# Kernel optimization log

Measured on AMD Instinct MI355X. Metric: run time of the kernel, lower is better.

Reference implementation:

```python
import jax, jax.numpy as jnp
import numpy as np
import math

B, A, I, O = 4096, 32, 256, 256


def setup_inputs() -> dict:
    key = jax.random.key(0)
    kx, kw, kb = jax.random.split(key, 3)
    x = jax.random.normal(kx, (B, A, I), dtype=jnp.float32)
    # kaiming_uniform_(a=sqrt(5)) on [A, O, I]: fan_in = I, bound = sqrt(6/((1+5)*I)) = 1/sqrt(I)
    wb = 1.0 / math.sqrt(I)
    weight = jax.random.uniform(kw, (A, O, I), minval=-wb, maxval=wb, dtype=jnp.float32)
    bb = 1.0 / math.sqrt(I)
    bias = jax.random.uniform(kb, (A, O), minval=-bb, maxval=bb, dtype=jnp.float32)
    return {"x": x, "weight": weight, "bias": bias}


def reference(x, weight, bias):
    # per-assignment batched GEMM: weight [A,O,I], x [B,A,I] -> [B,A,O]
    return jnp.einsum('aoi,bai->bao', weight, x) + bias
```

## Files before the change

### kernel.cpp

```cpp
#include <hip/hip_runtime.h>

typedef __attribute__((ext_vector_type(4))) float f32x4;
typedef __attribute__((ext_vector_type(2))) unsigned u32x2;
typedef __attribute__((ext_vector_type(8))) short bf16x8;

constexpr int Bsz = 4096, Asz = 32, Isz = 256, Osz = 256;
constexpr int NI = 16;

__device__ inline unsigned cvtpk(float lo, float hi) {
    unsigned r;
    asm("v_cvt_pk_bf16_f32 %0, %1, %2" : "=v"(r) : "v"(lo), "v"(hi));
    return r;
}

__global__ __launch_bounds__(512, 2) void al_gemm(const float* __restrict__ x,
                                                  const float* __restrict__ wsrc,
                                                  const float* __restrict__ bias,
                                                  float* __restrict__ out)
{
    __shared__ char sA[2][16384];
    __shared__ char sB[131072];

    const int p  = blockIdx.x;
    const int a  = (p & 7) * 4 + ((p >> 3) & 3);
    const int b0 = (p >> 5) * 512;

    const int t    = threadIdx.x;
    const int w    = t >> 6;
    const int lane = t & 63;
    const int llo  = lane & 15, lhi = lane >> 4;

    const float* fs[4];
    int wadr[4];
#pragma unroll
    for (int j = 0; j < 4; ++j) {
        const int lr = 4 * w + j;
        fs[j]   = x + ((size_t)(b0 + lr) * Asz + a) * Isz + lane * 4;
        wadr[j] = lr * 512 + (((lane >> 1) ^ lr) << 4) + (lane & 1) * 8;
    }
    const size_t STEP = (size_t)32 * Asz * Isz;

    f32x4 LA[4], LB[4];

#define FISSUE(Lset, tn) {                                                     \
    const size_t o_ = (size_t)(tn) * STEP;                                     \
    _Pragma("unroll")                                                          \
    for (int j = 0; j < 4; ++j) Lset[j] = *(const f32x4*)(fs[j] + o_);         \
    asm volatile("" : "+v"(Lset[0]), "+v"(Lset[1]), "+v"(Lset[2]), "+v"(Lset[3])); }

#define FWRITE(Lset, buf) {                                                    \
    char* Ad = &sA[buf][0];                                                    \
    _Pragma("unroll")                                                          \
    for (int j = 0; j < 4; ++j)                                                \
        *(u32x2*)&Ad[wadr[j]] =                                                \
            (u32x2){cvtpk(Lset[j][0], Lset[j][1]), cvtpk(Lset[j][2], Lset[j][3])}; }

    FISSUE(LA, 0);

    {
        const float* wa = wsrc + (size_t)a * (Osz * Isz);
#pragma unroll
        for (int i = 0; i < 16; ++i) {
            const int s     = i * 512 + t;
            const int o     = s >> 5;
            const int kt    = (s >> 2) & 7;
            const int nf    = s >> 9;
            const int lane_ = (o & 15) | ((s & 3) << 4);
            f32x4 lo = *(const f32x4*)(wa + (size_t)s * 8);
            f32x4 hi = *(const f32x4*)(wa + (size_t)s * 8 + 4);
            union { bf16x8 v; unsigned u[4]; } r;
            r.u[0] = cvtpk(lo[0], lo[1]); r.u[1] = cvtpk(lo[2], lo[3]);
            r.u[2] = cvtpk(hi[0], hi[1]); r.u[3] = cvtpk(hi[2], hi[3]);
            *(bf16x8*)&sB[(((kt * 16 + nf) * 64) + lane_) * 16] = r.v;
        }
    }

    const float bv0 = bias[a * Osz + w * 32 + llo];
    const float bv1 = bias[a * Osz + w * 32 + 16 + llo];

    FWRITE(LA, 0);
    FISSUE(LB, 1);

    __syncthreads();

    const int lr1 = llo + 16;

    auto COMPUTE_STORE = [&](const char* As, int tn) {
        f32x4 acc00 = (f32x4)(bv0), acc01 = (f32x4)(bv1);
        f32x4 acc10 = (f32x4)(bv0), acc11 = (f32x4)(bv1);
        __builtin_amdgcn_s_setprio(1);
#pragma unroll
        for (int kt = 0; kt < 8; ++kt) {
            const int c = kt * 4 + lhi;
            const bf16x8 aF0 = *(const bf16x8*)&As[llo * 512 + ((c ^ llo) << 4)];
            const bf16x8 aF1 = *(const bf16x8*)&As[lr1 * 512 + ((c ^ lr1) << 4)];
            const bf16x8 bF0 = *(const bf16x8*)&sB[(kt * 16 + 2 * w) * 1024 + lane * 16];
            const bf16x8 bF1 = *(const bf16x8*)&sB[(kt * 16 + 2 * w + 1) * 1024 + lane * 16];
            acc00 = __builtin_amdgcn_mfma_f32_16x16x32_bf16(aF0, bF0, acc00, 0, 0, 0);
            acc01 = __builtin_amdgcn_mfma_f32_16x16x32_bf16(aF0, bF1, acc01, 0, 0, 0);
            acc10 = __builtin_amdgcn_mfma_f32_16x16x32_bf16(aF1, bF0, acc10, 0, 0, 0);
            acc11 = __builtin_amdgcn_mfma_f32_16x16x32_bf16(aF1, bF1, acc11, 0, 0, 0);
        }
        __builtin_amdgcn_s_setprio(0);

        const int trow = b0 + tn * 32 + lhi * 4;
        float* op0 = out + ((size_t)trow * Asz + a) * Osz + w * 32 + llo;
        float* op1 = op0 + (size_t)16 * Asz * Osz;
#pragma unroll
        for (int r2 = 0; r2 < 4; ++r2) {
            op0[(size_t)r2 * Asz * Osz]      = acc00[r2];
            op0[(size_t)r2 * Asz * Osz + 16] = acc01[r2];
            op1[(size_t)r2 * Asz * Osz]      = acc10[r2];
            op1[(size_t)r2 * Asz * Osz + 16] = acc11[r2];
        }
    };

#pragma unroll
    for (int i = 0; i < NI / 2; ++i) {
        if (2 * i + 2 < NI) FISSUE(LA, 2 * i + 2);
        COMPUTE_STORE(&sA[0][0], 2 * i);
        FWRITE(LB, 1);
        asm volatile("s_waitcnt lgkmcnt(0)" ::: "memory");
        __builtin_amdgcn_s_barrier();

        if (2 * i + 3 < NI) FISSUE(LB, 2 * i + 3);
        COMPUTE_STORE(&sA[1][0], 2 * i + 1);
        if (2 * i + 2 < NI) {
            FWRITE(LA, 0);
            asm volatile("s_waitcnt lgkmcnt(0)" ::: "memory");
            __builtin_amdgcn_s_barrier();
        }
    }
#undef FISSUE
#undef FWRITE
}

extern "C" void kernel_launch(void* const* d_in, const int* in_sizes, int n_in,
                              void* d_out, int out_size, void* d_ws, size_t ws_size,
                              hipStream_t stream) {
    const float* x    = (const float*)d_in[0];
    const float* w    = (const float*)d_in[1];
    const float* bias = (const float*)d_in[2];
    float* out        = (float*)d_out;
    al_gemm<<<dim3(256), dim3(512), 0, stream>>>(x, w, bias, out);
}
```

Before: 56.27 us.

## Split output columns across two blocks with 256-thread blocks and 16-row tiles

The work is repartitioned so each block handles half of the O dimension (128 outputs) using 4 waves instead of 8. The grid doubles to 512 blocks and the batch tile per iteration shrinks from 32 to 16 rows. LDS use per block is halved, so more blocks can be resident and the 256 CUs are better covered. The cost is that every x tile is now loaded and converted twice, once per O-half, and each wave does fewer MFMAs per A-fragment load.

```diff
diff --git a/kernel.cpp b/kernel.cpp
--- a/kernel.cpp
+++ b/kernel.cpp
@@ -1,11 +1,11 @@
 #include <hip/hip_runtime.h>
 
 typedef __attribute__((ext_vector_type(4))) float f32x4;
-typedef __attribute__((ext_vector_type(2))) unsigned u32x2;
+typedef __attribute__((ext_vector_type(4))) unsigned u32x4;
 typedef __attribute__((ext_vector_type(8))) short bf16x8;
 
-constexpr int Bsz = 4096, Asz = 32, Isz = 256, Osz = 256;
-constexpr int NI = 16;
+constexpr int Asz = 32, Isz = 256, Osz = 256;
+constexpr int NI = 32;
 
 __device__ inline unsigned cvtpk(float lo, float hi) {
     unsigned r;
@@ -13,105 +13,97 @@
     return r;
 }
 
-__global__ __launch_bounds__(512, 2) void al_gemm(const float* __restrict__ x,
+__global__ __launch_bounds__(256, 2) void al_gemm(const float* __restrict__ x,
                                                   const float* __restrict__ wsrc,
                                                   const float* __restrict__ bias,
                                                   float* __restrict__ out)
 {
-    __shared__ char sA[2][16384];
-    __shared__ char sB[131072];
+    __shared__ char sA[2][8192];
+    __shared__ char sB[65536];
 
     const int p  = blockIdx.x;
-    const int a  = (p & 7) * 4 + ((p >> 3) & 3);
-    const int b0 = (p >> 5) * 512;
+    const int q  = p >> 3;
+    const int a  = (p & 7) * 4 + (q & 3);
+    const int b0 = ((q >> 2) & 7) * 512;
+    const int oh = q >> 5;
 
     const int t    = threadIdx.x;
     const int w    = t >> 6;
     const int lane = t & 63;
     const int llo  = lane & 15, lhi = lane >> 4;
 
-    const float* fs[4];
-    int wadr[4];
-#pragma unroll
-    for (int j = 0; j < 4; ++j) {
-        const int lr = 4 * w + j;
-        fs[j]   = x + ((size_t)(b0 + lr) * Asz + a) * Isz + lane * 4;
-        wadr[j] = lr * 512 + (((lane >> 1) ^ lr) << 4) + (lane & 1) * 8;
-    }
-    const size_t STEP = (size_t)32 * Asz * Isz;
+    const int frow = t >> 4;
+    const int c0   = (t & 15) * 2;
+    const float* xrow = x + ((size_t)(b0 + frow) * Asz + a) * Isz + (t & 15) * 16;
+    const int wadr0 = frow * 512 + ((c0       ^ frow) << 4);
+    const int wadr1 = frow * 512 + (((c0 + 1) ^ frow) << 4);
+    const size_t STEP = (size_t)16 * Asz * Isz;
 
     f32x4 LA[4], LB[4];
 
 #define FISSUE(Lset, tn) {                                                     \
-    const size_t o_ = (size_t)(tn) * STEP;                                     \
+    const float* nx = xrow + (size_t)(tn) * STEP;                              \
     _Pragma("unroll")                                                          \
-    for (int j = 0; j < 4; ++j) Lset[j] = *(const f32x4*)(fs[j] + o_);         \
+    for (int j = 0; j < 4; ++j) Lset[j] = *(const f32x4*)(nx + j * 4);         \
     asm volatile("" : "+v"(Lset[0]), "+v"(Lset[1]), "+v"(Lset[2]), "+v"(Lset[3])); }
 
 #define FWRITE(Lset, buf) {                                                    \
     char* Ad = &sA[buf][0];                                                    \
-    _Pragma("unroll")                                                          \
-    for (int j = 0; j < 4; ++j)                                                \
-        *(u32x2*)&Ad[wadr[j]] =                                                \
-            (u32x2){cvtpk(Lset[j][0], Lset[j][1]), cvtpk(Lset[j][2], Lset[j][3])}; }
+    u32x4 pk0, pk1;                                                            \
+    pk0[0] = cvtpk(Lset[0][0], Lset[0][1]); pk0[1] = cvtpk(Lset[0][2], Lset[0][3]); \
+    pk0[2] = cvtpk(Lset[1][0], Lset[1][1]); pk0[3] = cvtpk(Lset[1][2], Lset[1][3]); \
+    pk1[0] = cvtpk(Lset[2][0], Lset[2][1]); pk1[1] = cvtpk(Lset[2][2], Lset[2][3]); \
+    pk1[2] = cvtpk(Lset[3][0], Lset[3][1]); pk1[3] = cvtpk(Lset[3][2], Lset[3][3]); \
+    *(u32x4*)&Ad[wadr0] = pk0;                                                 \
+    *(u32x4*)&Ad[wadr1] = pk1; }
 
     FISSUE(LA, 0);
 
     {
-        const float* wa = wsrc + (size_t)a * (Osz * Isz);
+        const float* wa = wsrc + (size_t)a * (Osz * Isz) + (size_t)oh * 32768;
 #pragma unroll
         for (int i = 0; i < 16; ++i) {
-            const int s     = i * 512 + t;
-            const int o     = s >> 5;
+            const int s     = i * 256 + t;
+            const int o_l   = s >> 5;
             const int kt    = (s >> 2) & 7;
-            const int nf    = s >> 9;
-            const int lane_ = (o & 15) | ((s & 3) << 4);
+            const int nfl   = s >> 9;
+            const int lane_ = (o_l & 15) | ((s & 3) << 4);
             f32x4 lo = *(const f32x4*)(wa + (size_t)s * 8);
             f32x4 hi = *(const f32x4*)(wa + (size_t)s * 8 + 4);
             union { bf16x8 v; unsigned u[4]; } r;
             r.u[0] = cvtpk(lo[0], lo[1]); r.u[1] = cvtpk(lo[2], lo[3]);
             r.u[2] = cvtpk(hi[0], hi[1]); r.u[3] = cvtpk(hi[2], hi[3]);
-            *(bf16x8*)&sB[(((kt * 16 + nf) * 64) + lane_) * 16] = r.v;
+            *(bf16x8*)&sB[(((kt * 8 + nfl) * 64) + lane_) * 16] = r.v;
         }
     }
 
-    const float bv0 = bias[a * Osz + w * 32 + llo];
-    const float bv1 = bias[a * Osz + w * 32 + 16 + llo];
+    const float bv0 = bias[a * Osz + oh * 128 + w * 32 + llo];
+    const float bv1 = bias[a * Osz + oh * 128 + w * 32 + 16 + llo];
 
     FWRITE(LA, 0);
     FISSUE(LB, 1);
 
     __syncthreads();
 
-    const int lr1 = llo + 16;
-
     auto COMPUTE_STORE = [&](const char* As, int tn) {
-        f32x4 acc00 = (f32x4)(bv0), acc01 = (f32x4)(bv1);
-        f32x4 acc10 = (f32x4)(bv0), acc11 = (f32x4)(bv1);
+        f32x4 acc0 = (f32x4)(bv0), acc1 = (f32x4)(bv1);
         __builtin_amdgcn_s_setprio(1);
 #pragma unroll
         for (int kt = 0; kt < 8; ++kt) {
-            const int c = kt * 4 + lhi;
-            const bf16x8 aF0 = *(const bf16x8*)&As[llo * 512 + ((c ^ llo) << 4)];
-            const bf16x8 aF1 = *(const bf16x8*)&As[lr1 * 512 + ((c ^ lr1) << 4)];
-            const bf16x8 bF0 = *(const bf16x8*)&sB[(kt * 16 + 2 * w) * 1024 + lane * 16];
-            const bf16x8 bF1 = *(const bf16x8*)&sB[(kt * 16 + 2 * w + 1) * 1024 + lane * 16];
-            acc00 = __builtin_amdgcn_mfma_f32_16x16x32_bf16(aF0, bF0, acc00, 0, 0, 0);
-            acc01 = __builtin_amdgcn_mfma_f32_16x16x32_bf16(aF0, bF1, acc01, 0, 0, 0);
-            acc10 = __builtin_amdgcn_mfma_f32_16x16x32_bf16(aF1, bF0, acc10, 0, 0, 0);
-            acc11 = __builtin_amdgcn_mfma_f32_16x16x32_bf16(aF1, bF1, acc11, 0, 0, 0);
+            const bf16x8 aF  = *(const bf16x8*)&As[llo * 512 + (((kt * 4 + lhi) ^ llo) << 4)];
+            const bf16x8 bF0 = *(const bf16x8*)&sB[((kt * 8 + 2 * w) * 64 + lane) * 16];
+            const bf16x8 bF1 = *(const bf16x8*)&sB[((kt * 8 + 2 * w + 1) * 64 + lane) * 16];
+            acc0 = __builtin_amdgcn_mfma_f32_16x16x32_bf16(aF, bF0, acc0, 0, 0, 0);
+            acc1 = __builtin_amdgcn_mfma_f32_16x16x32_bf16(aF, bF1, acc1, 0, 0, 0);
         }
         __builtin_amdgcn_s_setprio(0);
 
-        const int trow = b0 + tn * 32 + lhi * 4;
-        float* op0 = out + ((size_t)trow * Asz + a) * Osz + w * 32 + llo;
-        float* op1 = op0 + (size_t)16 * Asz * Osz;
+        const int trow = b0 + tn * 16 + lhi * 4;
+        float* op = out + ((size_t)trow * Asz + a) * Osz + oh * 128 + w * 32 + llo;
 #pragma unroll
         for (int r2 = 0; r2 < 4; ++r2) {
-            op0[(size_t)r2 * Asz * Osz]      = acc00[r2];
-            op0[(size_t)r2 * Asz * Osz + 16] = acc01[r2];
-            op1[(size_t)r2 * Asz * Osz]      = acc10[r2];
-            op1[(size_t)r2 * Asz * Osz + 16] = acc11[r2];
+            op[(size_t)r2 * Asz * Osz]      = acc0[r2];
+            op[(size_t)r2 * Asz * Osz + 16] = acc1[r2];
         }
     };
 
@@ -142,5 +134,5 @@
     const float* w    = (const float*)d_in[1];
     const float* bias = (const float*)d_in[2];
     float* out        = (float*)d_out;
-    al_gemm<<<dim3(256), dim3(512), 0, stream>>>(x, w, bias, out);
+    al_gemm<<<dim3(512), dim3(256), 0, stream>>>(x, w, bias, out);
 }
```

After: 60.56 us. 7.6% more time.
